# Optimization experiments

Hardware: AMD Instinct MI355X
Metric: run time of the kernel (lower is better)

The kernel has to match this reference:

```python
import jax, jax.numpy as jnp
import numpy as np
from jax.ops import segment_sum, segment_max

N = 100000   # nodes
E = 1000000  # edges
G = 100      # graphs in batch
NF, EF = 9, 2
FT, FE = 3, 8
HID = 64
H, C = 4, 16          # heads, per-head channels (H*C == HID, concat=True)
LAT = 32
L = 3                 # num GAT layers
NEG_SLOPE = 0.2       # PyG GATConv LeakyReLU slope


def setup_inputs() -> dict:
    key = jax.random.key(0)
    ks = jax.random.split(key, 20)
    def nrm(k, shp, s=0.05):
        return jax.random.normal(k, shp, jnp.float32) * s
    return dict(
        x=jax.random.normal(ks[0], (N, NF), jnp.float32),
        face_types=jax.random.randint(ks[1], (N,), 0, FT),
        edge_index=jax.random.randint(ks[2], (2, E), 0, N),
        edge_attr=jax.random.normal(ks[3], (E, EF), jnp.float32),
        batch=jnp.sort(jax.random.randint(ks[4], (N,), 0, G)),
        node_mask=jnp.ones((N,), jnp.float32),
        num_graphs=G,
        face_emb=nrm(ks[5], (FT, FE)),
        node_W=nrm(ks[6], (NF + FE, HID)), node_b=jnp.zeros((HID,), jnp.float32),
        edge_W=nrm(ks[7], (EF, HID)), edge_b=jnp.zeros((HID,), jnp.float32),
        gat_lin=nrm(ks[8], (L, HID, HID)),
        gat_lin_edge=nrm(ks[9], (L, HID, HID)),
        gat_att_src=nrm(ks[10], (L, H, C)),
        gat_att_dst=nrm(ks[11], (L, H, C)),
        gat_att_edge=nrm(ks[12], (L, H, C)),
        gat_bias=jnp.zeros((L, HID), jnp.float32),
        mu_W=nrm(ks[13], (HID, LAT)), mu_b=jnp.zeros((LAT,), jnp.float32),
        lv_W=nrm(ks[14], (HID, LAT)), lv_b=jnp.zeros((LAT,), jnp.float32),
    )


def _gat(h, src, dst, edge_h, W, We, a_s, a_d, a_e, b):
    """PyG GATConv (eval): shared lin, self-loops with fill_value='mean', segment softmax over dst."""
    n = h.shape[0]
    xh = (h @ W).reshape(n, H, C)                       # (N,H,C)
    al_s = (xh * a_s).sum(-1)                           # (N,H)
    al_d = (xh * a_d).sum(-1)                           # (N,H)
    # self-loop edge_attr = mean of incoming encoded edge features (fill_value='mean')
    deg = segment_sum(jnp.ones((src.shape[0],), h.dtype), dst, num_segments=n)
    loop_attr = segment_sum(edge_h, dst, num_segments=n) / jnp.clip(deg, 1.0)[:, None]
    loops = jnp.arange(n)
    sa = jnp.concatenate([src, loops])                  # (E+N,)
    da = jnp.concatenate([dst, loops])
    ea = jnp.concatenate([edge_h, loop_attr], axis=0)   # (E+N,HID)
    eh = (ea @ We).reshape(-1, H, C)
    al_e = (eh * a_e).sum(-1)                           # (E+N,H)
    alpha = jax.nn.leaky_relu(al_s[sa] + al_d[da] + al_e, NEG_SLOPE)
    amax = segment_max(alpha, da, num_segments=n)       # every node has a self-loop -> no empty segment
    ex = jnp.exp(alpha - amax[da])
    denom = segment_sum(ex, da, num_segments=n)
    w = ex / denom[da]                                  # (E+N,H)
    out = segment_sum(xh[sa] * w[:, :, None], da, num_segments=n)  # (N,H,C)
    return out.reshape(n, H * C) + b


def reference(x, face_types, edge_index, edge_attr, batch, node_mask, num_graphs,
              face_emb, node_W, node_b, edge_W, edge_b,
              gat_lin, gat_lin_edge, gat_att_src, gat_att_dst, gat_att_edge, gat_bias,
              mu_W, mu_b, lv_W, lv_b):
    h = jax.nn.relu(jnp.concatenate([x, face_emb[face_types]], axis=-1) @ node_W + node_b)
    edge_h = jax.nn.relu(edge_attr @ edge_W + edge_b)
    src, dst = edge_index[0], edge_index[1]
    for l in range(gat_lin.shape[0]):
        h = jax.nn.relu(_gat(h, src, dst, edge_h, gat_lin[l], gat_lin_edge[l],
                             gat_att_src[l], gat_att_dst[l], gat_att_edge[l], gat_bias[l]))
    # masked scatter-mean pooling per graph
    hm = h * node_mask[:, None]
    h_sum = segment_sum(hm, batch, num_segments=num_graphs)
    counts = segment_sum(node_mask, batch, num_segments=num_graphs)
    hp = h_sum / jnp.clip(counts, 1.0)[:, None]
    mu = hp @ mu_W + mu_b
    logvar = hp @ lv_W + lv_b
    return mu, logvar
```

## Files before the change

kernel.cpp:

```cpp
#include <hip/hip_runtime.h>
#include <math.h>

#define NN 100000
#define NE 1000000
#define NG 100
#define NL 3
#define NEG 0.2f

__device__ __forceinline__ float lrelu(float x){ return fmaxf(x, NEG*x); }

__global__ void k_ve(const float* __restrict__ We, const float* __restrict__ ae,
                     float* __restrict__ Ve2){
  int i = blockIdx.x*blockDim.x + threadIdx.x;
  if(i >= NL*4*64) return;
  int d = i & 63, h = (i>>6)&3, l = i>>8;
  const float* w = We + l*4096 + d*64 + h*16;
  const float* a = ae + l*64 + h*16;
  float s = 0.f;
  #pragma unroll
  for(int c=0;c<16;c++) s = fmaf(w[c], a[c], s);
  Ve2[(l*4+h)*64 + d] = s;
}

__global__ void k_h0(const float* __restrict__ x, const int* __restrict__ ft,
                     const float* __restrict__ femb, const float* __restrict__ W,
                     const float* __restrict__ b, float* __restrict__ h){
  int i = blockIdx.x*blockDim.x + threadIdx.x;
  if(i >= NN*64) return;
  int n = i>>6, d = i&63;
  const float* xr = x + (size_t)n*9;
  const float* fe = femb + ft[n]*8;
  float s = b[d];
  #pragma unroll
  for(int k=0;k<9;k++) s = fmaf(xr[k], W[k*64+d], s);
  #pragma unroll
  for(int j=0;j<8;j++) s = fmaf(fe[j], W[(9+j)*64+d], s);
  h[i] = fmaxf(s, 0.f);
}

__global__ void k_deg(const int* __restrict__ dst, int* __restrict__ deg){
  int e = blockIdx.x*blockDim.x + threadIdx.x;
  if(e < NE) atomicAdd(&deg[dst[e]], 1);
}

__global__ void k_scan1(const int* __restrict__ deg, int* __restrict__ rp,
                        int* __restrict__ bsum){
  __shared__ int sd[256];
  int t = threadIdx.x;
  int base = blockIdx.x*1024 + t*4;
  int v0 = (base+0<NN)?deg[base+0]:0;
  int v1 = (base+1<NN)?deg[base+1]:0;
  int v2 = (base+2<NN)?deg[base+2]:0;
  int v3 = (base+3<NN)?deg[base+3]:0;
  int ts = v0+v1+v2+v3;
  sd[t] = ts; __syncthreads();
  for(int off=1; off<256; off<<=1){
    int add = (t>=off)? sd[t-off] : 0;
    __syncthreads();
    sd[t] += add;
    __syncthreads();
  }
  int excl = sd[t] - ts;
  if(t==255) bsum[blockIdx.x] = sd[t];
  if(base+0<NN) rp[base+0]=excl;
  if(base+1<NN) rp[base+1]=excl+v0;
  if(base+2<NN) rp[base+2]=excl+v0+v1;
  if(base+3<NN) rp[base+3]=excl+v0+v1+v2;
}
__global__ void k_scan2(int* __restrict__ bsum, int nb){
  if(threadIdx.x==0 && blockIdx.x==0){
    int acc=0;
    for(int i=0;i<nb;i++){ int v=bsum[i]; bsum[i]=acc; acc+=v; }
  }
}
__global__ void k_scan3(int* __restrict__ rp, const int* __restrict__ bsum){
  int i = blockIdx.x*blockDim.x + threadIdx.x;
  if(i < NN) rp[i] += bsum[i>>10];
  if(i == 0) rp[NN] = NE;
}

__global__ void k_scatter(const int* __restrict__ src, const int* __restrict__ dst,
                          const float* __restrict__ eattr, const int* __restrict__ rp,
                          int* __restrict__ fill, float4* __restrict__ ebuf){
  int e = blockIdx.x*blockDim.x + threadIdx.x;
  if(e >= NE) return;
  int dd = dst[e];
  int pos = rp[dd] + atomicAdd(&fill[dd], 1);
  float4 r;
  r.x = __int_as_float(src[e]);
  r.y = eattr[(size_t)e*2];
  r.z = eattr[(size_t)e*2+1];
  r.w = 0.f;
  ebuf[pos] = r;
}

__global__ void k_edge(const float4* __restrict__ ebuf, const float* __restrict__ eW,
                       const float* __restrict__ eb, const float* __restrict__ Ve2,
                       int* __restrict__ csrc, float* __restrict__ cal){
  int e = blockIdx.x*blockDim.x + threadIdx.x;
  if(e >= NE) return;
  float4 r = ebuf[e];
  int ss = __float_as_int(r.x);
  float a0 = r.y, a1 = r.z;
  float acc[12];
  #pragma unroll
  for(int t=0;t<12;t++) acc[t]=0.f;
  #pragma unroll 4
  for(int d=0; d<64; d+=4){
    float4 w0 = *(const float4*)&eW[d];
    float4 w1 = *(const float4*)&eW[64+d];
    float4 bb = *(const float4*)&eb[d];
    float4 eh;
    eh.x = fmaxf(fmaf(a0, w0.x, fmaf(a1, w1.x, bb.x)), 0.f);
    eh.y = fmaxf(fmaf(a0, w0.y, fmaf(a1, w1.y, bb.y)), 0.f);
    eh.z = fmaxf(fmaf(a0, w0.z, fmaf(a1, w1.z, bb.z)), 0.f);
    eh.w = fmaxf(fmaf(a0, w0.w, fmaf(a1, w1.w, bb.w)), 0.f);
    #pragma unroll
    for(int j=0;j<12;j++){
      float4 v = *(const float4*)&Ve2[j*64 + d];
      acc[j] = fmaf(eh.x, v.x, acc[j]);
      acc[j] = fmaf(eh.y, v.y, acc[j]);
      acc[j] = fmaf(eh.z, v.z, acc[j]);
      acc[j] = fmaf(eh.w, v.w, acc[j]);
    }
  }
  csrc[e] = ss;
  *(float4*)&cal[(size_t)e*4]          = make_float4(acc[0], acc[1], acc[2],  acc[3]);
  *(float4*)&cal[((size_t)NE   + e)*4] = make_float4(acc[4], acc[5], acc[6],  acc[7]);
  *(float4*)&cal[((size_t)NE*2 + e)*4] = make_float4(acc[8], acc[9], acc[10], acc[11]);
}

__global__ __launch_bounds__(256) void k_xh(
    const float* __restrict__ hin, const float* __restrict__ W,
    const float* __restrict__ aS, const float* __restrict__ aD,
    float* __restrict__ xh, float* __restrict__ alsd){
  __shared__ float hs[64][68];
  __shared__ float Ws[64][64];
  int t  = threadIdx.x;
  int td = t & 15;
  int tn = t >> 4;
  int n0 = blockIdx.x*64;
  size_t base = (size_t)n0*64;
  #pragma unroll
  for(int i=0;i<4;i++){
    int idx4 = t + i*256;
    int row  = idx4 >> 4;
    int c4   = (idx4 & 15)*4;
    float4 hv = make_float4(0.f,0.f,0.f,0.f);
    if(base + (size_t)idx4*4 < (size_t)NN*64)
      hv = *(const float4*)&hin[base + (size_t)idx4*4];
    *(float4*)&hs[row][c4] = hv;
    *(float4*)&Ws[row][c4] = *(const float4*)&W[(size_t)idx4*4];
  }
  __syncthreads();

  float acc[4][4];
  #pragma unroll
  for(int i=0;i<4;i++)
    #pragma unroll
    for(int j=0;j<4;j++) acc[i][j]=0.f;

  for(int k=0;k<64;k+=4){
    float4 w0 = *(float4*)&Ws[k+0][td*4];
    float4 w1 = *(float4*)&Ws[k+1][td*4];
    float4 w2 = *(float4*)&Ws[k+2][td*4];
    float4 w3 = *(float4*)&Ws[k+3][td*4];
    #pragma unroll
    for(int i=0;i<4;i++){
      float4 hv = *(float4*)&hs[tn*4+i][k];
      acc[i][0] = fmaf(hv.x, w0.x, acc[i][0]);
      acc[i][1] = fmaf(hv.x, w0.y, acc[i][1]);
      acc[i][2] = fmaf(hv.x, w0.z, acc[i][2]);
      acc[i][3] = fmaf(hv.x, w0.w, acc[i][3]);
      acc[i][0] = fmaf(hv.y, w1.x, acc[i][0]);
      acc[i][1] = fmaf(hv.y, w1.y, acc[i][1]);
      acc[i][2] = fmaf(hv.y, w1.z, acc[i][2]);
      acc[i][3] = fmaf(hv.y, w1.w, acc[i][3]);
      acc[i][0] = fmaf(hv.z, w2.x, acc[i][0]);
      acc[i][1] = fmaf(hv.z, w2.y, acc[i][1]);
      acc[i][2] = fmaf(hv.z, w2.z, acc[i][2]);
      acc[i][3] = fmaf(hv.z, w2.w, acc[i][3]);
      acc[i][0] = fmaf(hv.w, w3.x, acc[i][0]);
      acc[i][1] = fmaf(hv.w, w3.y, acc[i][1]);
      acc[i][2] = fmaf(hv.w, w3.z, acc[i][2]);
      acc[i][3] = fmaf(hv.w, w3.w, acc[i][3]);
    }
  }

  float as0 = aS[td*4+0], as1 = aS[td*4+1], as2 = aS[td*4+2], as3 = aS[td*4+3];
  float ad0 = aD[td*4+0], ad1 = aD[td*4+1], ad2 = aD[td*4+2], ad3 = aD[td*4+3];
  int head = td>>2;

  #pragma unroll
  for(int i=0;i<4;i++){
    int n = n0 + tn*4 + i;
    if(n >= NN) break;
    *(float4*)&xh[(size_t)n*64 + td*4] =
        make_float4(acc[i][0], acc[i][1], acc[i][2], acc[i][3]);
    float vs = acc[i][0]*as0 + acc[i][1]*as1 + acc[i][2]*as2 + acc[i][3]*as3;
    float vd = acc[i][0]*ad0 + acc[i][1]*ad1 + acc[i][2]*ad2 + acc[i][3]*ad3;
    vs += __shfl_xor(vs, 1); vs += __shfl_xor(vs, 2);
    vd += __shfl_xor(vd, 1); vd += __shfl_xor(vd, 2);
    if((td&3)==0){
      alsd[(size_t)n*8 + head]     = vs;
      alsd[(size_t)n*8 + 4 + head] = vd;
    }
  }
}

__global__ __launch_bounds__(256) void k_gat(
    const float* __restrict__ xh, const float* __restrict__ alsd,
    const int* __restrict__ rp, const int* __restrict__ csrc,
    const float* __restrict__ cal, const float* __restrict__ bias,
    float* __restrict__ hout){
  int d = threadIdx.x & 63, h = d>>4;
  int n = __builtin_amdgcn_readfirstlane(blockIdx.x*4 + (threadIdx.x>>6));
  if(n >= NN) return;
  int r0 = rp[n], r1 = rp[n+1];
  int dg = r1 - r0;
  float alD_n = alsd[(size_t)n*8 + 4 + h];
  float m = -1e30f, den = 0.f, acc = 0.f, sum_al = 0.f;
  int p = r0;
  for(; p+4 <= r1; p += 4){
    int s0 = csrc[p+0];
    int s1 = csrc[p+1];
    int s2 = csrc[p+2];
    int s3 = csrc[p+3];
    float e0 = cal[(size_t)(p+0)*4 + h];
    float e1 = cal[(size_t)(p+1)*4 + h];
    float e2 = cal[(size_t)(p+2)*4 + h];
    float e3 = cal[(size_t)(p+3)*4 + h];
    float a0 = alsd[(size_t)s0*8 + h];
    float a1 = alsd[(size_t)s1*8 + h];
    float a2 = alsd[(size_t)s2*8 + h];
    float a3 = alsd[(size_t)s3*8 + h];
    float x0 = xh[(size_t)s0*64 + d];
    float x1 = xh[(size_t)s1*64 + d];
    float x2 = xh[(size_t)s2*64 + d];
    float x3 = xh[(size_t)s3*64 + d];
    sum_al += e0 + e1 + e2 + e3;
    float l0 = lrelu(a0 + alD_n + e0);
    float l1 = lrelu(a1 + alD_n + e1);
    float l2 = lrelu(a2 + alD_n + e2);
    float l3 = lrelu(a3 + alD_n + e3);
    float pmax = fmaxf(fmaxf(l0, l1), fmaxf(l2, l3));
    if(pmax > m + 8.f){
      float sc = __expf(m - pmax);
      den *= sc; acc *= sc; m = pmax;
    }
    float w0 = __expf(l0 - m); den += w0; acc = fmaf(w0, x0, acc);
    float w1 = __expf(l1 - m); den += w1; acc = fmaf(w1, x1, acc);
    float w2 = __expf(l2 - m); den += w2; acc = fmaf(w2, x2, acc);
    float w3 = __expf(l3 - m); den += w3; acc = fmaf(w3, x3, acc);
  }
  for(; p < r1; p++){
    int s = csrc[p];
    float e = cal[(size_t)p*4 + h];
    float as = alsd[(size_t)s*8 + h];
    float xv = xh[(size_t)s*64 + d];
    sum_al += e;
    float lg = lrelu(as + alD_n + e);
    if(lg > m + 8.f){
      float sc = __expf(m - lg);
      den *= sc; acc *= sc; m = lg;
    }
    float w = __expf(lg - m); den += w; acc = fmaf(w, xv, acc);
  }
  float alS_n = alsd[(size_t)n*8 + h];
  float loop_al = dg>0 ? sum_al/(float)dg : 0.f;
  float la = lrelu(alS_n + alD_n + loop_al);
  float nm = fmaxf(m, la);
  float sc = __expf(m - nm);
  float wl = __expf(la - nm);
  den = den*sc + wl;
  acc = fmaf(wl, xh[(size_t)n*64+d], acc*sc);
  hout[(size_t)n*64+d] = fmaxf(acc/den + bias[d], 0.f);
}

__global__ void k_pool(const float* __restrict__ h, const int* __restrict__ batch,
                       const float* __restrict__ mask, float* __restrict__ hsum,
                       float* __restrict__ cnt){
  int d = threadIdx.x;
  int start = blockIdx.x*64;
  if(start >= NN) return;
  int end = min(start+64, NN);
  int curg = batch[start];
  float acc = 0.f, c = 0.f;
  for(int n=start; n<end; n++){
    int g = batch[n];
    if(g != curg){
      atomicAdd(&hsum[(size_t)curg*64+d], acc);
      if(d==0) atomicAdd(&cnt[curg], c);
      acc = 0.f; c = 0.f; curg = g;
    }
    float mk = mask[n];
    acc = fmaf(h[(size_t)n*64+d], mk, acc);
    if(d==0) c += mk;
  }
  atomicAdd(&hsum[(size_t)curg*64+d], acc);
  if(d==0) atomicAdd(&cnt[curg], c);
}

__global__ void k_final(const float* __restrict__ hsum, const float* __restrict__ cnt,
                        const float* __restrict__ muW, const float* __restrict__ mub,
                        const float* __restrict__ lvW, const float* __restrict__ lvb,
                        float* __restrict__ out){
  int i = blockIdx.x*blockDim.x + threadIdx.x;
  if(i >= NG*32*2) return;
  int which = i / (NG*32);
  int r = i % (NG*32);
  int g = r >> 5, j = r & 31;
  float rc = 1.f / fmaxf(cnt[g], 1.f);
  const float* W = which ? lvW : muW;
  float s = which ? lvb[j] : mub[j];
  const float* hr = hsum + (size_t)g*64;
  #pragma unroll 8
  for(int k=0;k<64;k++) s = fmaf(hr[k]*rc, W[k*32+j], s);
  out[i] = s;
}

extern "C" void kernel_launch(void* const* d_in, const int* in_sizes, int n_in,
                              void* d_out, int out_size, void* d_ws, size_t ws_size,
                              hipStream_t stream){
  const float* x      = (const float*)d_in[0];
  const int*   ft     = (const int*)d_in[1];
  const int*   ei     = (const int*)d_in[2];
  const float* eattr  = (const float*)d_in[3];
  const int*   batch  = (const int*)d_in[4];
  const float* mask   = (const float*)d_in[5];
  const float* femb   = (const float*)d_in[7];
  const float* nW     = (const float*)d_in[8];
  const float* nb     = (const float*)d_in[9];
  const float* eW     = (const float*)d_in[10];
  const float* ebias  = (const float*)d_in[11];
  const float* glin   = (const float*)d_in[12];
  const float* gline  = (const float*)d_in[13];
  const float* aS     = (const float*)d_in[14];
  const float* aD     = (const float*)d_in[15];
  const float* aE     = (const float*)d_in[16];
  const float* gbias  = (const float*)d_in[17];
  const float* muW    = (const float*)d_in[18];
  const float* mub    = (const float*)d_in[19];
  const float* lvW    = (const float*)d_in[20];
  const float* lvb    = (const float*)d_in[21];
  const int* src = ei;
  const int* dstp = ei + NE;

  char* ws = (char*)d_ws;
  size_t off = 0;
  auto alloc = [&](size_t bytes)->void*{
    void* p = ws + off; off += (bytes + 255) & ~(size_t)255; return p;
  };
  int*    deg   = (int*)   alloc((size_t)NN*4);
  int*    fill  = (int*)   alloc((size_t)NN*4);
  int*    rp    = (int*)   alloc((size_t)(NN+1)*4);
  int*    bsum  = (int*)   alloc(128*4);
  float4* ebuf  = (float4*)alloc((size_t)NE*16);
  int*    csrc  = (int*)   alloc((size_t)NE*4);
  float*  cal   = (float*) alloc((size_t)NL*NE*4*4);
  float*  alsd  = (float*) alloc((size_t)NN*8*4);
  float*  Ve2   = (float*) alloc((size_t)NL*4*64*4);
  float*  hbuf  = (float*) alloc((size_t)NN*64*4);
  float*  xb    = (float*) alloc((size_t)NN*64*4);
  float*  hsum  = (float*) alloc((size_t)NG*64*4);
  float*  cnt   = (float*) alloc((size_t)NG*4);

  hipMemsetAsync(deg,  0, (size_t)NN*4, stream);
  hipMemsetAsync(fill, 0, (size_t)NN*4, stream);
  hipMemsetAsync(hsum, 0, (size_t)NG*64*4, stream);
  hipMemsetAsync(cnt,  0, (size_t)NG*4, stream);

  k_ve  <<<3, 256, 0, stream>>>(gline, aE, Ve2);
  k_h0  <<<(NN*64+255)/256, 256, 0, stream>>>(x, ft, femb, nW, nb, hbuf);
  k_deg <<<(NE+255)/256, 256, 0, stream>>>(dstp, deg);
  k_scan1<<<(NN+1023)/1024, 256, 0, stream>>>(deg, rp, bsum);
  k_scan2<<<1, 64, 0, stream>>>(bsum, (NN+1023)/1024);
  k_scan3<<<(NN+255)/256, 256, 0, stream>>>(rp, bsum);
  k_scatter<<<(NE+255)/256, 256, 0, stream>>>(src, dstp, eattr, rp, fill, ebuf);
  k_edge<<<(NE+255)/256, 256, 0, stream>>>(ebuf, eW, ebias, Ve2, csrc, cal);

  for(int l=0;l<NL;l++){
    k_xh <<<(NN+63)/64, 256, 0, stream>>>(hbuf, glin + (size_t)l*4096,
                                          aS + l*64, aD + l*64, xb, alsd);
    k_gat<<<(NN+3)/4, 256, 0, stream>>>(xb, alsd, rp, csrc,
                                        cal + (size_t)l*NE*4, gbias + l*64, hbuf);
  }
  k_pool <<<(NN+63)/64, 64, 0, stream>>>(hbuf, batch, mask, hsum, cnt);
  k_final<<<(NG*32*2+255)/256, 256, 0, stream>>>(hsum, cnt, muW, mub, lvW, lvb,
                                                 (float*)d_out);
}
```

Measured before the change: 465.7 us.

## Split edge scatter into pack and permutation, widen GAT gather unroll

Replaces the scatter that wrote 16-byte records to random CSR positions with a coalesced pack kernel plus a permutation kernel that scatters only 4-byte edge ids. Each thread now handles four strided edges, giving more independent atomics in flight. The edge kernel then gathers packed records through the permutation. The GAT aggregation loop is unrolled from 4 to 8 neighbors to expose more independent gathers. This adds an extra pass and a random gather in k_edge, and raises register pressure in k_gat.

```diff
diff --git a/kernel.cpp b/kernel.cpp
--- a/kernel.cpp
+++ b/kernel.cpp
@@ -39,8 +39,13 @@
 }
 
 __global__ void k_deg(const int* __restrict__ dst, int* __restrict__ deg){
-  int e = blockIdx.x*blockDim.x + threadIdx.x;
-  if(e < NE) atomicAdd(&deg[dst[e]], 1);
+  int i = blockIdx.x*blockDim.x + threadIdx.x;
+  if(i >= NE/4) return;
+  #pragma unroll
+  for(int k=0;k<4;k++){
+    int e = i + k*(NE/4);
+    atomicAdd(&deg[dst[e]], 1);
+  }
 }
 
 __global__ void k_scan1(const int* __restrict__ deg, int* __restrict__ rp,
@@ -79,27 +84,42 @@
   if(i == 0) rp[NN] = NE;
 }
 
-__global__ void k_scatter(const int* __restrict__ src, const int* __restrict__ dst,
-                          const float* __restrict__ eattr, const int* __restrict__ rp,
-                          int* __restrict__ fill, float4* __restrict__ ebuf){
+__global__ void k_pack(const int* __restrict__ src, const float* __restrict__ eattr,
+                       float4* __restrict__ pack){
   int e = blockIdx.x*blockDim.x + threadIdx.x;
   if(e >= NE) return;
-  int dd = dst[e];
-  int pos = rp[dd] + atomicAdd(&fill[dd], 1);
   float4 r;
   r.x = __int_as_float(src[e]);
   r.y = eattr[(size_t)e*2];
   r.z = eattr[(size_t)e*2+1];
   r.w = 0.f;
-  ebuf[pos] = r;
-}
-
-__global__ void k_edge(const float4* __restrict__ ebuf, const float* __restrict__ eW,
-                       const float* __restrict__ eb, const float* __restrict__ Ve2,
+  pack[e] = r;
+}
+
+__global__ void k_perm(const int* __restrict__ dst, const int* __restrict__ rp,
+                       int* __restrict__ fill, int* __restrict__ perm){
+  int i = blockIdx.x*blockDim.x + threadIdx.x;
+  if(i >= NE/4) return;
+  int e0 = i, e1 = i + (NE/4), e2 = i + 2*(NE/4), e3 = i + 3*(NE/4);
+  int d0 = dst[e0], d1 = dst[e1], d2 = dst[e2], d3 = dst[e3];
+  int p0 = rp[d0] + atomicAdd(&fill[d0], 1);
+  int p1 = rp[d1] + atomicAdd(&fill[d1], 1);
+  int p2 = rp[d2] + atomicAdd(&fill[d2], 1);
+  int p3 = rp[d3] + atomicAdd(&fill[d3], 1);
+  perm[p0] = e0;
+  perm[p1] = e1;
+  perm[p2] = e2;
+  perm[p3] = e3;
+}
+
+__global__ void k_edge(const int* __restrict__ perm, const float4* __restrict__ pack,
+                       const float* __restrict__ eW, const float* __restrict__ eb,
+                       const float* __restrict__ Ve2,
                        int* __restrict__ csrc, float* __restrict__ cal){
   int e = blockIdx.x*blockDim.x + threadIdx.x;
   if(e >= NE) return;
-  float4 r = ebuf[e];
+  int eid = perm[e];
+  float4 r = pack[eid];
   int ss = __float_as_int(r.x);
   float a0 = r.y, a1 = r.z;
   float acc[12];
@@ -221,37 +241,34 @@
   float alD_n = alsd[(size_t)n*8 + 4 + h];
   float m = -1e30f, den = 0.f, acc = 0.f, sum_al = 0.f;
   int p = r0;
-  for(; p+4 <= r1; p += 4){
-    int s0 = csrc[p+0];
-    int s1 = csrc[p+1];
-    int s2 = csrc[p+2];
-    int s3 = csrc[p+3];
-    float e0 = cal[(size_t)(p+0)*4 + h];
-    float e1 = cal[(size_t)(p+1)*4 + h];
-    float e2 = cal[(size_t)(p+2)*4 + h];
-    float e3 = cal[(size_t)(p+3)*4 + h];
-    float a0 = alsd[(size_t)s0*8 + h];
-    float a1 = alsd[(size_t)s1*8 + h];
-    float a2 = alsd[(size_t)s2*8 + h];
-    float a3 = alsd[(size_t)s3*8 + h];
-    float x0 = xh[(size_t)s0*64 + d];
-    float x1 = xh[(size_t)s1*64 + d];
-    float x2 = xh[(size_t)s2*64 + d];
-    float x3 = xh[(size_t)s3*64 + d];
-    sum_al += e0 + e1 + e2 + e3;
-    float l0 = lrelu(a0 + alD_n + e0);
-    float l1 = lrelu(a1 + alD_n + e1);
-    float l2 = lrelu(a2 + alD_n + e2);
-    float l3 = lrelu(a3 + alD_n + e3);
-    float pmax = fmaxf(fmaxf(l0, l1), fmaxf(l2, l3));
+  for(; p+8 <= r1; p += 8){
+    int   s[8]; float e[8]; float a[8]; float x[8];
+    #pragma unroll
+    for(int k=0;k<8;k++) s[k] = csrc[p+k];
+    #pragma unroll
+    for(int k=0;k<8;k++) e[k] = cal[(size_t)(p+k)*4 + h];
+    #pragma unroll
+    for(int k=0;k<8;k++) a[k] = alsd[(size_t)s[k]*8 + h];
+    #pragma unroll
+    for(int k=0;k<8;k++) x[k] = xh[(size_t)s[k]*64 + d];
+    float lg[8];
+    float pmax = -1e30f;
+    #pragma unroll
+    for(int k=0;k<8;k++){
+      sum_al += e[k];
+      lg[k] = lrelu(a[k] + alD_n + e[k]);
+      pmax = fmaxf(pmax, lg[k]);
+    }
     if(pmax > m + 8.f){
       float sc = __expf(m - pmax);
       den *= sc; acc *= sc; m = pmax;
     }
-    float w0 = __expf(l0 - m); den += w0; acc = fmaf(w0, x0, acc);
-    float w1 = __expf(l1 - m); den += w1; acc = fmaf(w1, x1, acc);
-    float w2 = __expf(l2 - m); den += w2; acc = fmaf(w2, x2, acc);
-    float w3 = __expf(l3 - m); den += w3; acc = fmaf(w3, x3, acc);
+    #pragma unroll
+    for(int k=0;k<8;k++){
+      float w = __expf(lg[k] - m);
+      den += w;
+      acc = fmaf(w, x[k], acc);
+    }
   }
   for(; p < r1; p++){
     int s = csrc[p];
@@ -355,7 +372,8 @@
   int*    fill  = (int*)   alloc((size_t)NN*4);
   int*    rp    = (int*)   alloc((size_t)(NN+1)*4);
   int*    bsum  = (int*)   alloc(128*4);
-  float4* ebuf  = (float4*)alloc((size_t)NE*16);
+  int*    perm  = (int*)   alloc((size_t)NE*4);
+  float4* pack  = (float4*)alloc((size_t)NE*16);
   int*    csrc  = (int*)   alloc((size_t)NE*4);
   float*  cal   = (float*) alloc((size_t)NL*NE*4*4);
   float*  alsd  = (float*) alloc((size_t)NN*8*4);
@@ -372,12 +390,13 @@
 
   k_ve  <<<3, 256, 0, stream>>>(gline, aE, Ve2);
   k_h0  <<<(NN*64+255)/256, 256, 0, stream>>>(x, ft, femb, nW, nb, hbuf);
-  k_deg <<<(NE+255)/256, 256, 0, stream>>>(dstp, deg);
+  k_deg <<<(NE/4+255)/256, 256, 0, stream>>>(dstp, deg);
   k_scan1<<<(NN+1023)/1024, 256, 0, stream>>>(deg, rp, bsum);
   k_scan2<<<1, 64, 0, stream>>>(bsum, (NN+1023)/1024);
   k_scan3<<<(NN+255)/256, 256, 0, stream>>>(rp, bsum);
-  k_scatter<<<(NE+255)/256, 256, 0, stream>>>(src, dstp, eattr, rp, fill, ebuf);
-  k_edge<<<(NE+255)/256, 256, 0, stream>>>(ebuf, eW, ebias, Ve2, csrc, cal);
+  k_pack<<<(NE+255)/256, 256, 0, stream>>>(src, eattr, pack);
+  k_perm<<<(NE/4+255)/256, 256, 0, stream>>>(dstp, rp, fill, perm);
+  k_edge<<<(NE+255)/256, 256, 0, stream>>>(perm, pack, eW, ebias, Ve2, csrc, cal);
 
   for(int l=0;l<NL;l++){
     k_xh <<<(NN+63)/64, 256, 0, stream>>>(hbuf, glin + (size_t)l*4096,
```

Result: slower. 491.0 us (+5.4%).

## Record atomic rank in degree pass and fuse CSR scatter into edge kernel

Applied to the files above, without the earlier changes.

The degree-count kernel now stores each edge's atomicAdd return value as its rank within its destination bucket. This removes the separate scatter kernel, its fill counter and the intermediate ebuf array. The edge-feature kernel reads edge attributes in their original order and writes its results directly to the CSR position rp[dst]+rank. The pooling kernel also packs four 64-node chunks into each 256-thread block. The cost is an extra rank array and scattered, uncoalesced writes of three float4s per edge, and the order of edges within each CSR segment stays nondeterministic.

```diff
diff --git a/kernel.cpp b/kernel.cpp
--- a/kernel.cpp
+++ b/kernel.cpp
@@ -38,9 +38,15 @@
   h[i] = fmaxf(s, 0.f);
 }
 
-__global__ void k_deg(const int* __restrict__ dst, int* __restrict__ deg){
-  int e = blockIdx.x*blockDim.x + threadIdx.x;
-  if(e < NE) atomicAdd(&deg[dst[e]], 1);
+__global__ void k_deg(const int* __restrict__ dst, int* __restrict__ deg,
+                      int* __restrict__ rank){
+  int i = blockIdx.x*blockDim.x + threadIdx.x;
+  if(i >= NE/4) return;
+  #pragma unroll
+  for(int k=0;k<4;k++){
+    int e = i + k*(NE/4);
+    rank[e] = atomicAdd(&deg[dst[e]], 1);
+  }
 }
 
 __global__ void k_scan1(const int* __restrict__ deg, int* __restrict__ rp,
@@ -79,29 +85,14 @@
   if(i == 0) rp[NN] = NE;
 }
 
-__global__ void k_scatter(const int* __restrict__ src, const int* __restrict__ dst,
-                          const float* __restrict__ eattr, const int* __restrict__ rp,
-                          int* __restrict__ fill, float4* __restrict__ ebuf){
-  int e = blockIdx.x*blockDim.x + threadIdx.x;
-  if(e >= NE) return;
-  int dd = dst[e];
-  int pos = rp[dd] + atomicAdd(&fill[dd], 1);
-  float4 r;
-  r.x = __int_as_float(src[e]);
-  r.y = eattr[(size_t)e*2];
-  r.z = eattr[(size_t)e*2+1];
-  r.w = 0.f;
-  ebuf[pos] = r;
-}
-
-__global__ void k_edge(const float4* __restrict__ ebuf, const float* __restrict__ eW,
-                       const float* __restrict__ eb, const float* __restrict__ Ve2,
+__global__ void k_edge(const float* __restrict__ eattr, const int* __restrict__ src,
+                       const int* __restrict__ dst, const int* __restrict__ rank,
+                       const float* __restrict__ eW, const float* __restrict__ eb,
+                       const float* __restrict__ Ve2, const int* __restrict__ rp,
                        int* __restrict__ csrc, float* __restrict__ cal){
   int e = blockIdx.x*blockDim.x + threadIdx.x;
   if(e >= NE) return;
-  float4 r = ebuf[e];
-  int ss = __float_as_int(r.x);
-  float a0 = r.y, a1 = r.z;
+  float a0 = eattr[(size_t)e*2], a1 = eattr[(size_t)e*2+1];
   float acc[12];
   #pragma unroll
   for(int t=0;t<12;t++) acc[t]=0.f;
@@ -124,10 +115,12 @@
       acc[j] = fmaf(eh.w, v.w, acc[j]);
     }
   }
-  csrc[e] = ss;
-  *(float4*)&cal[(size_t)e*4]          = make_float4(acc[0], acc[1], acc[2],  acc[3]);
-  *(float4*)&cal[((size_t)NE   + e)*4] = make_float4(acc[4], acc[5], acc[6],  acc[7]);
-  *(float4*)&cal[((size_t)NE*2 + e)*4] = make_float4(acc[8], acc[9], acc[10], acc[11]);
+  int dd = dst[e];
+  int pos = rp[dd] + rank[e];
+  csrc[pos] = src[e];
+  *(float4*)&cal[(size_t)pos*4]          = make_float4(acc[0], acc[1], acc[2],  acc[3]);
+  *(float4*)&cal[((size_t)NE   + pos)*4] = make_float4(acc[4], acc[5], acc[6],  acc[7]);
+  *(float4*)&cal[((size_t)NE*2 + pos)*4] = make_float4(acc[8], acc[9], acc[10], acc[11]);
 }
 
 __global__ __launch_bounds__(256) void k_xh(
@@ -277,11 +270,12 @@
   hout[(size_t)n*64+d] = fmaxf(acc/den + bias[d], 0.f);
 }
 
-__global__ void k_pool(const float* __restrict__ h, const int* __restrict__ batch,
-                       const float* __restrict__ mask, float* __restrict__ hsum,
-                       float* __restrict__ cnt){
-  int d = threadIdx.x;
-  int start = blockIdx.x*64;
+__global__ __launch_bounds__(256) void k_pool(
+    const float* __restrict__ h, const int* __restrict__ batch,
+    const float* __restrict__ mask, float* __restrict__ hsum,
+    float* __restrict__ cnt){
+  int d = threadIdx.x & 63;
+  int start = blockIdx.x*256 + (threadIdx.x>>6)*64;
   if(start >= NN) return;
   int end = min(start+64, NN);
   int curg = batch[start];
@@ -352,10 +346,9 @@
     void* p = ws + off; off += (bytes + 255) & ~(size_t)255; return p;
   };
   int*    deg   = (int*)   alloc((size_t)NN*4);
-  int*    fill  = (int*)   alloc((size_t)NN*4);
+  int*    rank  = (int*)   alloc((size_t)NE*4);
   int*    rp    = (int*)   alloc((size_t)(NN+1)*4);
   int*    bsum  = (int*)   alloc(128*4);
-  float4* ebuf  = (float4*)alloc((size_t)NE*16);
   int*    csrc  = (int*)   alloc((size_t)NE*4);
   float*  cal   = (float*) alloc((size_t)NL*NE*4*4);
   float*  alsd  = (float*) alloc((size_t)NN*8*4);
@@ -366,18 +359,17 @@
   float*  cnt   = (float*) alloc((size_t)NG*4);
 
   hipMemsetAsync(deg,  0, (size_t)NN*4, stream);
-  hipMemsetAsync(fill, 0, (size_t)NN*4, stream);
   hipMemsetAsync(hsum, 0, (size_t)NG*64*4, stream);
   hipMemsetAsync(cnt,  0, (size_t)NG*4, stream);
 
   k_ve  <<<3, 256, 0, stream>>>(gline, aE, Ve2);
   k_h0  <<<(NN*64+255)/256, 256, 0, stream>>>(x, ft, femb, nW, nb, hbuf);
-  k_deg <<<(NE+255)/256, 256, 0, stream>>>(dstp, deg);
+  k_deg <<<(NE/4+255)/256, 256, 0, stream>>>(dstp, deg, rank);
   k_scan1<<<(NN+1023)/1024, 256, 0, stream>>>(deg, rp, bsum);
   k_scan2<<<1, 64, 0, stream>>>(bsum, (NN+1023)/1024);
   k_scan3<<<(NN+255)/256, 256, 0, stream>>>(rp, bsum);
-  k_scatter<<<(NE+255)/256, 256, 0, stream>>>(src, dstp, eattr, rp, fill, ebuf);
-  k_edge<<<(NE+255)/256, 256, 0, stream>>>(ebuf, eW, ebias, Ve2, csrc, cal);
+  k_edge<<<(NE+255)/256, 256, 0, stream>>>(eattr, src, dstp, rank, eW, ebias,
+                                           Ve2, rp, csrc, cal);
 
   for(int l=0;l<NL;l++){
     k_xh <<<(NN+63)/64, 256, 0, stream>>>(hbuf, glin + (size_t)l*4096,
@@ -385,7 +377,7 @@
     k_gat<<<(NN+3)/4, 256, 0, stream>>>(xb, alsd, rp, csrc,
                                         cal + (size_t)l*NE*4, gbias + l*64, hbuf);
   }
-  k_pool <<<(NN+63)/64, 64, 0, stream>>>(hbuf, batch, mask, hsum, cnt);
+  k_pool <<<(NN+255)/256, 256, 0, stream>>>(hbuf, batch, mask, hsum, cnt);
   k_final<<<(NG*32*2+255)/256, 256, 0, stream>>>(hsum, cnt, muW, mub, lvW, lvb,
                                                  (float*)d_out);
 }
```

New measurement: 428.9 us. 1.09x faster.
